# Optimization experiments

Measured on AMD Instinct MI355X. Metric: run time of the kernel, lower is better.

The kernel has to match this reference:

```python
import jax, jax.numpy as jnp
import numpy as np

N_NODES = 100000
N_EDGES = 1600000
IN_FEATS = 64
OUT_FEATS = 64


def setup_inputs() -> dict:
    key = jax.random.key(0)
    k1, k2, k3, k4, k5 = jax.random.split(key, 5)
    h = jax.random.normal(k1, (N_NODES, IN_FEATS), dtype=jnp.float32)
    weight = jax.random.normal(k2, (IN_FEATS, OUT_FEATS), dtype=jnp.float32) * (1.0 / np.sqrt(OUT_FEATS))
    norm = jax.random.uniform(k3, (N_NODES, 1), dtype=jnp.float32)
    src = jax.random.randint(k4, (N_EDGES,), 0, N_NODES, dtype=jnp.int32)
    dst = jax.random.randint(k5, (N_EDGES,), 0, N_NODES, dtype=jnp.int32)
    return {"h": h, "weight": weight, "norm": norm, "src": src, "dst": dst}


def reference(h, weight, norm, src, dst):
    # GCN linear: [N, in] @ [in, out] -> [N, out]
    hw = jnp.matmul(h, weight)
    # pre-scale by source norm
    hn = hw * norm
    # gather messages at edge sources, scatter-sum into destinations
    msgs = hn[src]  # [E, out]
    agg = jax.ops.segment_sum(msgs, dst, num_segments=h.shape[0])
    # post-scale by destination norm
    return agg * norm
```

## Files before the change

kernel.cpp:

```cpp
#include <hip/hip_runtime.h>

#define N_NODES 100000
#define N_EDGES 1600000
#define F 64
#define NPB 128
#define NB ((N_NODES + NPB - 1) / NPB)
#define CAP 2432
#define BLK_E 8192
#define NSPLIT ((N_EDGES + BLK_E - 1) / BLK_E)
#define GEMM_ROWS 64
#define NGEMM ((N_NODES + GEMM_ROWS - 1) / GEMM_ROWS)

typedef unsigned short ushort_t;
typedef unsigned int uint_t;
using bf16x8 = __attribute__((ext_vector_type(8))) short;
using f32x4  = __attribute__((ext_vector_type(4))) float;

__device__ __forceinline__ ushort_t f2bf(float x) {
    uint_t u = __float_as_uint(x);
    u += 0x7FFFu + ((u >> 16) & 1u);
    return (ushort_t)(u >> 16);
}
__device__ __forceinline__ float bflo(uint_t v) {
    return __uint_as_float(v << 16);
}
__device__ __forceinline__ float bfhi(uint_t v) {
    return __uint_as_float(v & 0xFFFF0000u);
}

__launch_bounds__(256)
__global__ void gemm_split_kernel(const float* __restrict__ h,
                                  const float* __restrict__ w,
                                  const float* __restrict__ norm,
                                  ushort_t* __restrict__ hn,
                                  const int* __restrict__ src,
                                  const int* __restrict__ dst,
                                  ushort_t* __restrict__ offtab,
                                  uint_t* __restrict__ seg) {
    __shared__ int hist[1024];
    __shared__ int cur[NB + 2];
    __shared__ int sc[256];
    const int t = threadIdx.x;

    if (blockIdx.x < NSPLIT) {
        const int e0 = blockIdx.x * BLK_E;
        const int n  = min(BLK_E, N_EDGES - e0);

        for (int i = t; i < 1024; i += 256) hist[i] = 0;
        __syncthreads();

        for (int i = t; i < n; i += 256)
            atomicAdd(&hist[dst[e0 + i] >> 7], 1);
        __syncthreads();

        const int b0i = 4 * t;
        int v0 = hist[b0i], v1 = hist[b0i + 1], v2 = hist[b0i + 2], v3 = hist[b0i + 3];
        const int ssum = v0 + v1 + v2 + v3;
        sc[t] = ssum;
        __syncthreads();
        int acc = ssum;
#pragma unroll
        for (int off = 1; off < 256; off <<= 1) {
            const int add = (t >= off) ? sc[t - off] : 0;
            __syncthreads();
            acc += add;
            sc[t] = acc;
            __syncthreads();
        }
        int run = acc - ssum;
        ushort_t* offrow = offtab + (size_t)blockIdx.x * (NB + 1);
        const int vj[4] = {v0, v1, v2, v3};
#pragma unroll
        for (int j = 0; j < 4; ++j) {
            const int bin = b0i + j;
            if (bin < NB) {
                offrow[bin] = (ushort_t)run;
                cur[bin] = run;
            } else if (bin == NB) {
                offrow[NB] = (ushort_t)run;
            }
            run += vj[j];
        }
        __syncthreads();

        uint_t* myseg = seg + (size_t)blockIdx.x * BLK_E;
        for (int i = t; i < n; i += 256) {
            const int d = dst[e0 + i];
            const int s = src[e0 + i];
            const int p = atomicAdd(&cur[d >> 7], 1);
            myseg[p] = ((uint_t)s << 7) | (uint_t)(d & 127);
        }
    } else {
        const int gb  = blockIdx.x - NSPLIT;
        const int wv  = t >> 6;
        const int l   = t & 63;
        const int lr  = l & 15;
        const int lk  = l >> 4;
        const int col = wv * 16 + lr;
        const int r0  = gb * GEMM_ROWS;

        bf16x8 b0, b1;
#pragma unroll
        for (int j = 0; j < 8; ++j) {
            b0[j] = (short)f2bf(w[(lk * 8 + j) * F + col]);
            b1[j] = (short)f2bf(w[(32 + lk * 8 + j) * F + col]);
        }

#pragma unroll
        for (int tt = 0; tt < 4; ++tt) {
            const int r  = r0 + tt * 16 + lr;
            const int rl = min(r, N_NODES - 1);
            const float4 ha0 = *(const float4*)(h + (size_t)rl * F + lk * 8);
            const float4 ha1 = *(const float4*)(h + (size_t)rl * F + lk * 8 + 4);
            const float4 hb0 = *(const float4*)(h + (size_t)rl * F + 32 + lk * 8);
            const float4 hb1 = *(const float4*)(h + (size_t)rl * F + 32 + lk * 8 + 4);
            bf16x8 a0, a1;
            a0[0] = (short)f2bf(ha0.x); a0[1] = (short)f2bf(ha0.y);
            a0[2] = (short)f2bf(ha0.z); a0[3] = (short)f2bf(ha0.w);
            a0[4] = (short)f2bf(ha1.x); a0[5] = (short)f2bf(ha1.y);
            a0[6] = (short)f2bf(ha1.z); a0[7] = (short)f2bf(ha1.w);
            a1[0] = (short)f2bf(hb0.x); a1[1] = (short)f2bf(hb0.y);
            a1[2] = (short)f2bf(hb0.z); a1[3] = (short)f2bf(hb0.w);
            a1[4] = (short)f2bf(hb1.x); a1[5] = (short)f2bf(hb1.y);
            a1[6] = (short)f2bf(hb1.z); a1[7] = (short)f2bf(hb1.w);

            f32x4 acc = {0.f, 0.f, 0.f, 0.f};
            acc = __builtin_amdgcn_mfma_f32_16x16x32_bf16(a0, b0, acc, 0, 0, 0);
            acc = __builtin_amdgcn_mfma_f32_16x16x32_bf16(a1, b1, acc, 0, 0, 0);

#pragma unroll
            for (int i2 = 0; i2 < 4; ++i2) {
                const int m = r0 + tt * 16 + lk * 4 + i2;
                if (m < N_NODES)
                    hn[(size_t)m * F + col] = f2bf(acc[i2] * norm[m]);
            }
        }
    }
}

__launch_bounds__(512)
__global__ void gather_build_kernel(const ushort_t* __restrict__ offtab,
                                    const uint_t* __restrict__ seg,
                                    const ushort_t* __restrict__ hn,
                                    const float* __restrict__ norm,
                                    float* __restrict__ out) {
    __shared__ uint_t ebuf[CAP];
    __shared__ int    lsrc[CAP];
    __shared__ int    cnt[NPB];
    __shared__ int    beg[NPB];
    __shared__ int    cur[NPB];
    __shared__ int    sc[NPB];
    __shared__ int    sstart[256];
    __shared__ int    scn[256];

    const int b = blockIdx.x;
    const int t = threadIdx.x;

    int slen_v = 0, sstart_v = 0;
    if (t < NSPLIT) {
        const ushort_t* row = offtab + (size_t)t * (NB + 1);
        sstart_v = row[b];
        slen_v   = row[b + 1] - sstart_v;
    }
    if (t < 256) { sstart[t] = sstart_v; scn[t] = slen_v; }
    __syncthreads();

    int acc = slen_v;
#pragma unroll
    for (int off = 1; off < 256; off <<= 1) {
        int add = 0;
        if (t < 256 && t >= off) add = scn[t - off];
        __syncthreads();
        if (t < 256) { acc += add; scn[t] = acc; }
        __syncthreads();
    }
    const int n = min(scn[255], CAP);

    const int wave = t >> 6;
    const int lane = t & 63;
    for (int s = wave; s < NSPLIT; s += 8) {
        const int base = scn[s] - (scn[s] - ((s > 0) ? scn[s - 1] : 0));
        const int len  = scn[s] - ((s > 0) ? scn[s - 1] : 0);
        const uint_t* sp = seg + (size_t)s * BLK_E + sstart[s];
        for (int j = lane; j < len; j += 64) {
            const int o = base + j;
            if (o < CAP) ebuf[o] = sp[j];
        }
    }
    __syncthreads();

    if (t < NPB) cnt[t] = 0;
    __syncthreads();
    for (int i = t; i < n; i += 512)
        atomicAdd(&cnt[ebuf[i] & 127u], 1);
    __syncthreads();

    int acc2 = (t < NPB) ? cnt[t] : 0;
    if (t < NPB) sc[t] = acc2;
    __syncthreads();
#pragma unroll
    for (int off = 1; off < NPB; off <<= 1) {
        int add = 0;
        if (t < NPB && t >= off) add = sc[t - off];
        __syncthreads();
        if (t < NPB) { acc2 += add; sc[t] = acc2; }
        __syncthreads();
    }
    if (t < NPB) {
        const int e = acc2 - cnt[t];
        beg[t] = e;
        cur[t] = e;
    }
    __syncthreads();

    for (int i = t; i < n; i += 512) {
        const uint_t e = ebuf[i];
        const int p = atomicAdd(&cur[e & 127u], 1);
        lsrc[p] = (int)(e >> 7);
    }
    __syncthreads();

    const int s = lane >> 4;
    const int c = lane & 15;

    for (int ld = wave; ld < NPB; ld += 8) {
        const int node = b * NPB + ld;
        if (node >= N_NODES) break;

        const int bg = beg[ld];
        const int en = bg + cnt[ld];

        float a0 = 0.f, a1 = 0.f, a2 = 0.f, a3 = 0.f;
        int i = bg;
        for (; i + 7 < en; i += 8) {
            const int sA = lsrc[i + s];
            const int sB = lsrc[i + 4 + s];
            const uint2 vA = *(const uint2*)(hn + (size_t)sA * F + 4 * c);
            const uint2 vB = *(const uint2*)(hn + (size_t)sB * F + 4 * c);
            a0 += bflo(vA.x) + bflo(vB.x);
            a1 += bfhi(vA.x) + bfhi(vB.x);
            a2 += bflo(vA.y) + bflo(vB.y);
            a3 += bfhi(vA.y) + bfhi(vB.y);
        }
        for (; i < en; i += 4) {
            const int e = i + s;
            if (e < en) {
                const int sv = lsrc[e];
                const uint2 v = *(const uint2*)(hn + (size_t)sv * F + 4 * c);
                a0 += bflo(v.x);
                a1 += bfhi(v.x);
                a2 += bflo(v.y);
                a3 += bfhi(v.y);
            }
        }

        a0 += __shfl_xor(a0, 16); a0 += __shfl_xor(a0, 32);
        a1 += __shfl_xor(a1, 16); a1 += __shfl_xor(a1, 32);
        a2 += __shfl_xor(a2, 16); a2 += __shfl_xor(a2, 32);
        a3 += __shfl_xor(a3, 16); a3 += __shfl_xor(a3, 32);

        if (s == 0) {
            const float nv = norm[node];
            float4 r;
            r.x = a0 * nv; r.y = a1 * nv; r.z = a2 * nv; r.w = a3 * nv;
            *(float4*)(out + (size_t)node * F + 4 * c) = r;
        }
    }
}

extern "C" void kernel_launch(void* const* d_in, const int* in_sizes, int n_in,
                              void* d_out, int out_size, void* d_ws, size_t ws_size,
                              hipStream_t stream) {
    const float* h    = (const float*)d_in[0];
    const float* w    = (const float*)d_in[1];
    const float* norm = (const float*)d_in[2];
    const int*   src  = (const int*)d_in[3];
    const int*   dst  = (const int*)d_in[4];
    float* out = (float*)d_out;

    char* ws = (char*)d_ws;
    ushort_t* hn     = (ushort_t*)ws;
    uint_t*   seg    = (uint_t*)(ws + 12800000);
    ushort_t* offtab = (ushort_t*)(ws + 12800000 + 6422528);

    gemm_split_kernel<<<NSPLIT + NGEMM, 256, 0, stream>>>(
        h, w, norm, hn, src, dst, offtab, seg);

    gather_build_kernel<<<NB, 512, 0, stream>>>(offtab, seg, hn, norm, out);
}
```

Baseline: 84.10 us.

## Halve edge split size, cache edge records in registers, restructure segment gather

The edge split block size drops from 8192 to 4096, so there are twice as many splits. Each thread now reads src/dst once and keeps the packed records in registers for both the histogram and the scatter pass, instead of rereading dst and src. In the gather kernel the per-split scan widens to 512 entries. Each split's segment is copied by a single thread, which also fills the per-node count histogram in the same pass, removing a separate pass and a barrier. The GEMM path batches its h loads before compute, and the aggregation loop is unrolled to 16 edges to raise memory-level parallelism. The serial per-thread segment copy and the larger offset table may add latency.

New measurement: 85.63 us. Within noise of the previous version (+1.8%).

```diff
diff --git a/kernel.cpp b/kernel.cpp
--- a/kernel.cpp
+++ b/kernel.cpp
@@ -6,8 +6,9 @@
 #define NPB 128
 #define NB ((N_NODES + NPB - 1) / NPB)
 #define CAP 2432
-#define BLK_E 8192
+#define BLK_E 4096
 #define NSPLIT ((N_EDGES + BLK_E - 1) / BLK_E)
+#define EPT (BLK_E / 256)
 #define GEMM_ROWS 64
 #define NGEMM ((N_NODES + GEMM_ROWS - 1) / GEMM_ROWS)
 
@@ -49,12 +50,26 @@
         for (int i = t; i < 1024; i += 256) hist[i] = 0;
         __syncthreads();
 
-        for (int i = t; i < n; i += 256)
-            atomicAdd(&hist[dst[e0 + i] >> 7], 1);
+        uint_t rec[EPT];
+        short  bin[EPT];
+#pragma unroll
+        for (int j = 0; j < EPT; ++j) {
+            const int idx = t + j * 256;
+            if (idx < n) {
+                const int d = dst[e0 + idx];
+                const int s = src[e0 + idx];
+                bin[j] = (short)(d >> 7);
+                rec[j] = ((uint_t)s << 7) | (uint_t)(d & 127);
+                atomicAdd(&hist[bin[j]], 1);
+            } else {
+                bin[j] = -1;
+            }
+        }
         __syncthreads();
 
         const int b0i = 4 * t;
-        int v0 = hist[b0i], v1 = hist[b0i + 1], v2 = hist[b0i + 2], v3 = hist[b0i + 3];
+        const int v0 = hist[b0i], v1 = hist[b0i + 1];
+        const int v2 = hist[b0i + 2], v3 = hist[b0i + 3];
         const int ssum = v0 + v1 + v2 + v3;
         sc[t] = ssum;
         __syncthreads();
@@ -72,11 +87,11 @@
         const int vj[4] = {v0, v1, v2, v3};
 #pragma unroll
         for (int j = 0; j < 4; ++j) {
-            const int bin = b0i + j;
-            if (bin < NB) {
-                offrow[bin] = (ushort_t)run;
-                cur[bin] = run;
-            } else if (bin == NB) {
+            const int b = b0i + j;
+            if (b < NB) {
+                offrow[b] = (ushort_t)run;
+                cur[b] = run;
+            } else if (b == NB) {
                 offrow[NB] = (ushort_t)run;
             }
             run += vj[j];
@@ -84,11 +99,12 @@
         __syncthreads();
 
         uint_t* myseg = seg + (size_t)blockIdx.x * BLK_E;
-        for (int i = t; i < n; i += 256) {
-            const int d = dst[e0 + i];
-            const int s = src[e0 + i];
-            const int p = atomicAdd(&cur[d >> 7], 1);
-            myseg[p] = ((uint_t)s << 7) | (uint_t)(d & 127);
+#pragma unroll
+        for (int j = 0; j < EPT; ++j) {
+            if (bin[j] >= 0) {
+                const int p = atomicAdd(&cur[bin[j]], 1);
+                myseg[p] = rec[j];
+            }
         }
     } else {
         const int gb  = blockIdx.x - NSPLIT;
@@ -106,33 +122,44 @@
             b1[j] = (short)f2bf(w[(32 + lk * 8 + j) * F + col]);
         }
 
+        float4 hv[4][4];
 #pragma unroll
         for (int tt = 0; tt < 4; ++tt) {
             const int r  = r0 + tt * 16 + lr;
             const int rl = min(r, N_NODES - 1);
-            const float4 ha0 = *(const float4*)(h + (size_t)rl * F + lk * 8);
-            const float4 ha1 = *(const float4*)(h + (size_t)rl * F + lk * 8 + 4);
-            const float4 hb0 = *(const float4*)(h + (size_t)rl * F + 32 + lk * 8);
-            const float4 hb1 = *(const float4*)(h + (size_t)rl * F + 32 + lk * 8 + 4);
+            const float* hp = h + (size_t)rl * F + lk * 8;
+            hv[tt][0] = *(const float4*)(hp);
+            hv[tt][1] = *(const float4*)(hp + 4);
+            hv[tt][2] = *(const float4*)(hp + 32);
+            hv[tt][3] = *(const float4*)(hp + 36);
+        }
+
+        f32x4 accv[4];
+#pragma unroll
+        for (int tt = 0; tt < 4; ++tt) {
             bf16x8 a0, a1;
-            a0[0] = (short)f2bf(ha0.x); a0[1] = (short)f2bf(ha0.y);
-            a0[2] = (short)f2bf(ha0.z); a0[3] = (short)f2bf(ha0.w);
-            a0[4] = (short)f2bf(ha1.x); a0[5] = (short)f2bf(ha1.y);
-            a0[6] = (short)f2bf(ha1.z); a0[7] = (short)f2bf(ha1.w);
-            a1[0] = (short)f2bf(hb0.x); a1[1] = (short)f2bf(hb0.y);
-            a1[2] = (short)f2bf(hb0.z); a1[3] = (short)f2bf(hb0.w);
-            a1[4] = (short)f2bf(hb1.x); a1[5] = (short)f2bf(hb1.y);
-            a1[6] = (short)f2bf(hb1.z); a1[7] = (short)f2bf(hb1.w);
+            a0[0] = (short)f2bf(hv[tt][0].x); a0[1] = (short)f2bf(hv[tt][0].y);
+            a0[2] = (short)f2bf(hv[tt][0].z); a0[3] = (short)f2bf(hv[tt][0].w);
+            a0[4] = (short)f2bf(hv[tt][1].x); a0[5] = (short)f2bf(hv[tt][1].y);
+            a0[6] = (short)f2bf(hv[tt][1].z); a0[7] = (short)f2bf(hv[tt][1].w);
+            a1[0] = (short)f2bf(hv[tt][2].x); a1[1] = (short)f2bf(hv[tt][2].y);
+            a1[2] = (short)f2bf(hv[tt][2].z); a1[3] = (short)f2bf(hv[tt][2].w);
+            a1[4] = (short)f2bf(hv[tt][3].x); a1[5] = (short)f2bf(hv[tt][3].y);
+            a1[6] = (short)f2bf(hv[tt][3].z); a1[7] = (short)f2bf(hv[tt][3].w);
 
             f32x4 acc = {0.f, 0.f, 0.f, 0.f};
             acc = __builtin_amdgcn_mfma_f32_16x16x32_bf16(a0, b0, acc, 0, 0, 0);
             acc = __builtin_amdgcn_mfma_f32_16x16x32_bf16(a1, b1, acc, 0, 0, 0);
-
+            accv[tt] = acc;
+        }
+
+#pragma unroll
+        for (int tt = 0; tt < 4; ++tt) {
 #pragma unroll
             for (int i2 = 0; i2 < 4; ++i2) {
                 const int m = r0 + tt * 16 + lk * 4 + i2;
                 if (m < N_NODES)
-                    hn[(size_t)m * F + col] = f2bf(acc[i2] * norm[m]);
+                    hn[(size_t)m * F + col] = f2bf(accv[tt][i2] * norm[m]);
             }
         }
     }
@@ -150,8 +177,8 @@
     __shared__ int    beg[NPB];
     __shared__ int    cur[NPB];
     __shared__ int    sc[NPB];
-    __shared__ int    sstart[256];
-    __shared__ int    scn[256];
+    __shared__ int    sstart[NSPLIT];
+    __shared__ int    scn[512];
 
     const int b = blockIdx.x;
     const int t = threadIdx.x;
@@ -161,38 +188,35 @@
         const ushort_t* row = offtab + (size_t)t * (NB + 1);
         sstart_v = row[b];
         slen_v   = row[b + 1] - sstart_v;
-    }
-    if (t < 256) { sstart[t] = sstart_v; scn[t] = slen_v; }
+        sstart[t] = sstart_v;
+    }
+    if (t < NPB) cnt[t] = 0;
+    scn[t] = slen_v;
     __syncthreads();
 
     int acc = slen_v;
 #pragma unroll
-    for (int off = 1; off < 256; off <<= 1) {
-        int add = 0;
-        if (t < 256 && t >= off) add = scn[t - off];
-        __syncthreads();
-        if (t < 256) { acc += add; scn[t] = acc; }
-        __syncthreads();
-    }
-    const int n = min(scn[255], CAP);
-
-    const int wave = t >> 6;
-    const int lane = t & 63;
-    for (int s = wave; s < NSPLIT; s += 8) {
-        const int base = scn[s] - (scn[s] - ((s > 0) ? scn[s - 1] : 0));
-        const int len  = scn[s] - ((s > 0) ? scn[s - 1] : 0);
-        const uint_t* sp = seg + (size_t)s * BLK_E + sstart[s];
-        for (int j = lane; j < len; j += 64) {
+    for (int off = 1; off < 512; off <<= 1) {
+        const int add = (t >= off) ? scn[t - off] : 0;
+        __syncthreads();
+        acc += add;
+        scn[t] = acc;
+        __syncthreads();
+    }
+    const int n = min(scn[511], CAP);
+
+    if (t < NSPLIT && slen_v > 0) {
+        const int base = acc - slen_v;
+        const uint_t* sp = seg + (size_t)t * BLK_E + sstart_v;
+        for (int j = 0; j < slen_v; ++j) {
             const int o = base + j;
-            if (o < CAP) ebuf[o] = sp[j];
-        }
-    }
-    __syncthreads();
-
-    if (t < NPB) cnt[t] = 0;
-    __syncthreads();
-    for (int i = t; i < n; i += 512)
-        atomicAdd(&cnt[ebuf[i] & 127u], 1);
+            if (o < CAP) {
+                const uint_t v = sp[j];
+                ebuf[o] = v;
+                atomicAdd(&cnt[v & 127u], 1);
+            }
+        }
+    }
     __syncthreads();
 
     int acc2 = (t < NPB) ? cnt[t] : 0;
@@ -220,6 +244,8 @@
     }
     __syncthreads();
 
+    const int wave = t >> 6;
+    const int lane = t & 63;
     const int s = lane >> 4;
     const int c = lane & 15;
 
@@ -232,15 +258,19 @@
 
         float a0 = 0.f, a1 = 0.f, a2 = 0.f, a3 = 0.f;
         int i = bg;
-        for (; i + 7 < en; i += 8) {
+        for (; i + 15 < en; i += 16) {
             const int sA = lsrc[i + s];
             const int sB = lsrc[i + 4 + s];
+            const int sC = lsrc[i + 8 + s];
+            const int sD = lsrc[i + 12 + s];
             const uint2 vA = *(const uint2*)(hn + (size_t)sA * F + 4 * c);
             const uint2 vB = *(const uint2*)(hn + (size_t)sB * F + 4 * c);
-            a0 += bflo(vA.x) + bflo(vB.x);
-            a1 += bfhi(vA.x) + bfhi(vB.x);
-            a2 += bflo(vA.y) + bflo(vB.y);
-            a3 += bfhi(vA.y) + bfhi(vB.y);
+            const uint2 vC = *(const uint2*)(hn + (size_t)sC * F + 4 * c);
+            const uint2 vD = *(const uint2*)(hn + (size_t)sD * F + 4 * c);
+            a0 += bflo(vA.x) + bflo(vB.x) + bflo(vC.x) + bflo(vD.x);
+            a1 += bfhi(vA.x) + bfhi(vB.x) + bfhi(vC.x) + bfhi(vD.x);
+            a2 += bflo(vA.y) + bflo(vB.y) + bflo(vC.y) + bflo(vD.y);
+            a3 += bfhi(vA.y) + bfhi(vB.y) + bfhi(vC.y) + bfhi(vD.y);
         }
         for (; i < en; i += 4) {
             const int e = i + s;
@@ -281,7 +311,7 @@
     char* ws = (char*)d_ws;
     ushort_t* hn     = (ushort_t*)ws;
     uint_t*   seg    = (uint_t*)(ws + 12800000);
-    ushort_t* offtab = (ushort_t*)(ws + 12800000 + 6422528);
+    ushort_t* offtab = (ushort_t*)(ws + 12800000 + 6406144);
 
     gemm_split_kernel<<<NSPLIT + NGEMM, 256, 0, stream>>>(
         h, w, norm, hn, src, dst, offtab, seg);
```
